# Optimization experiments

Measured on AMD Instinct MI355X. Metric: run time of the kernel, lower is better.

Reference implementation:

```python
import jax, jax.numpy as jnp
import numpy as np

N, E, EE = 1024, 32768, 262144
C_S, C_Z, C_G, H, R = 384, 128, 16, 4, 64
EPS = 1e-8


def _rbf(d, D_count=R, D_min=0.0, D_max=20.0):
    # gvp-style radial basis: exp(-((d - mu)/sigma)^2), mu in linspace(D_min, D_max)
    mu = jnp.linspace(D_min, D_max, D_count, dtype=d.dtype)
    sigma = (D_max - D_min) / D_count
    return jnp.exp(-(((d[..., None] - mu) / sigma) ** 2))


def _layernorm(x, g, b, eps=1e-5):
    m = jnp.mean(x, axis=-1, keepdims=True)
    v = jnp.var(x, axis=-1, keepdims=True)
    return (x - m) * jax.lax.rsqrt(v + eps) * g + b


def setup_inputs() -> dict:
    key = jax.random.key(0)
    ks = jax.random.split(key, 32)
    s = 0.02
    inp = {
        'node_features': jax.random.normal(ks[0], (N, C_S), jnp.float32),
        'node_trans': jax.random.normal(ks[1], (N, 3), jnp.float32) * 10.0,
        'edge_features': jax.random.normal(ks[2], (E, C_Z), jnp.float32),
        'edge_index': jax.random.randint(ks[3], (2, E), 0, N),
        'edge_edge_index': jax.random.randint(ks[4], (2, EE), 0, E),
        # layer norm
        'ln_g': jnp.ones((C_Z,), jnp.float32),
        'ln_b': jnp.zeros((C_Z,), jnp.float32),
        # node_left / node_right
        'W_nl': jax.random.normal(ks[5], (C_S, C_G), jnp.float32) * s,
        'b_nl': jnp.zeros((C_G,), jnp.float32),
        'W_nr': jax.random.normal(ks[6], (C_S, C_G), jnp.float32) * s,
        'b_nr': jnp.zeros((C_G,), jnp.float32),
        # bias_gate: (c_gate_s^2 -> c_z)
        'W_bg': jax.random.normal(ks[7], (C_G * C_G, C_Z), jnp.float32) * s,
        'b_bg': jnp.zeros((C_Z,), jnp.float32),
        # dist_bias: (num_rbf -> c_z)
        'W_db': jax.random.normal(ks[8], (R, C_Z), jnp.float32) * s,
        'b_db': jnp.zeros((C_Z,), jnp.float32),
        # to_bias: (c_z -> num_heads), no bias
        'W_tb': jax.random.normal(ks[9], (C_Z, H), jnp.float32) * s,
        # q / kv
        'W_q': jax.random.normal(ks[10], (C_Z, C_Z), jnp.float32) * s,
        'b_q': jnp.zeros((C_Z,), jnp.float32),
        'W_kv': jax.random.normal(ks[11], (C_Z, 2 * C_Z), jnp.float32) * s,
        'b_kv': jnp.zeros((2 * C_Z,), jnp.float32),
        # out gate + out proj
        'W_og': jax.random.normal(ks[12], (C_Z, C_Z), jnp.float32) * s,
        'b_og': jnp.zeros((C_Z,), jnp.float32),
        'W_out': jax.random.normal(ks[13], (C_Z, C_Z), jnp.float32) * s,
        'b_out': jnp.zeros((C_Z,), jnp.float32),
    }
    return inp


def reference(node_features, node_trans, edge_features, edge_index, edge_edge_index,
              ln_g, ln_b, W_nl, b_nl, W_nr, b_nr, W_bg, b_bg, W_db, b_db, W_tb,
              W_q, b_q, W_kv, b_kv, W_og, b_og, W_out, b_out):
    d = C_Z // H
    ee0, ee1 = edge_edge_index[0], edge_edge_index[1]
    # node indices of the two triangle corner nodes for each edge-edge pair
    n1 = edge_index[0, ee1]  # [EE]
    n2 = edge_index[0, ee0]  # [EE]

    ef = _layernorm(edge_features, ln_g, ln_b)  # [E, c_z]

    nl = node_features @ W_nl + b_nl  # [N, c_g]
    nr = node_features @ W_nr + b_nr
    # outer product gate features per edge-edge pair
    e3 = jnp.einsum('bi,bj->bij', nl[n1], nr[n2]).reshape(-1, C_G * C_G)  # [EE, c_g^2]
    gate = e3 @ W_bg + b_bg  # [EE, c_z]

    dist = jnp.linalg.norm(node_trans[n1] - node_trans[n2] + EPS, axis=-1)  # [EE]
    dist_bias = _rbf(dist) @ W_db + b_db  # [EE, c_z]
    bias = (jax.nn.sigmoid(gate) * dist_bias) @ W_tb  # [EE, H]

    q = (ef @ W_q + b_q).reshape(E, H, d)
    kv = ef @ W_kv + b_kv
    k = kv[:, :C_Z].reshape(E, H, d)
    v = kv[:, C_Z:].reshape(E, H, d)

    attn = jnp.einsum('bhi,bhi->bh', q[ee1], k[ee0]) * (1.0 / np.sqrt(C_Z)) + bias  # [EE, H]

    # segment softmax over target edge ee1
    seg_max = jax.ops.segment_max(attn, ee1, num_segments=E)  # [E, H]
    p = jnp.exp(attn - seg_max[ee1])
    seg_sum = jax.ops.segment_sum(p, ee1, num_segments=E)
    p = p / (seg_sum[ee1] + 1e-16)

    upd = jax.ops.segment_sum(v[ee0] * p[..., None], ee1, num_segments=E)  # [E, H, d]
    upd = upd.reshape(E, C_Z)
    upd = upd * jax.nn.sigmoid(ef @ W_og + b_og)
    return upd @ W_out + b_out
```

## Files before the change

kernel.cpp:

```cpp
#include <hip/hip_runtime.h>
#include <math.h>

#define NN 1024
#define NE 32768
#define NEE 262144
#define CS 384
#define CZ 128
#define CG 16
#define NH 4
#define NR 64

typedef __attribute__((ext_vector_type(8))) short short8v;
typedef __attribute__((ext_vector_type(4))) float f32x4;
typedef unsigned short ushort_t;

__device__ __forceinline__ float sigmoidf_(float x) { return 1.0f / (1.0f + __expf(-x)); }

__device__ __forceinline__ ushort_t f2bf(float x) {
    union { float f; unsigned u; } v; v.f = x;
    unsigned r = v.u + 0x7fff + ((v.u >> 16) & 1);
    return (ushort_t)(r >> 16);
}
__device__ __forceinline__ float bf2f(ushort_t x) {
    union { unsigned u; float f; } v; v.u = ((unsigned)x) << 16;
    return v.f;
}

__global__ void node_proj_kernel(const float* __restrict__ nf,
                                 const float* __restrict__ Wl, const float* __restrict__ bl,
                                 const float* __restrict__ Wr, const float* __restrict__ br,
                                 ushort_t* __restrict__ nl16, float* __restrict__ nr) {
    int wave = threadIdx.x >> 6, lane = threadIdx.x & 63;
    int n = blockIdx.x * 4 + wave;
    if (lane >= 32) return;
    bool isl = lane < 16;
    int o = isl ? lane : lane - 16;
    const float* W = isl ? Wl : Wr;
    float acc = isl ? bl[o] : br[o];
    const float* x = nf + n * CS;
    for (int k = 0; k < CS; ++k) acc += x[k] * W[k * 16 + o];
    if (isl) nl16[n * 16 + o] = f2bf(acc);
    else     nr[n * 16 + o] = acc;
}

__global__ void build_Tt_kernel(const float* __restrict__ nr, const float* __restrict__ Wbg,
                                ushort_t* __restrict__ Tbf) {
    int n = blockIdx.x;
    int t = threadIdx.x;
    int c = t & 127, i0 = t >> 7;
    __shared__ float nrs[16];
    if (t < 16) nrs[t] = nr[n * 16 + t];
    __syncthreads();
    for (int i = i0; i < 16; i += 2) {
        float acc = 0.f;
#pragma unroll
        for (int j = 0; j < 16; ++j) acc += nrs[j] * Wbg[(i * 16 + j) * 128 + c];
        Tbf[n * 2048 + c * 16 + i] = f2bf(acc);
    }
}

__global__ void ln_kernel(const float* __restrict__ x, const float* __restrict__ g,
                          const float* __restrict__ b, ushort_t* __restrict__ ef) {
    int wave = threadIdx.x >> 6, lane = threadIdx.x & 63;
    int e = blockIdx.x * 4 + wave;
    int c0 = lane, c1 = lane + 64;
    float x0 = x[e * 128 + c0], x1 = x[e * 128 + c1];
    float s = x0 + x1;
#pragma unroll
    for (int m = 1; m < 64; m <<= 1) s += __shfl_xor(s, m);
    float mean = s * (1.f / 128.f);
    float d0 = x0 - mean, d1 = x1 - mean;
    float v = d0 * d0 + d1 * d1;
#pragma unroll
    for (int m = 1; m < 64; m <<= 1) v += __shfl_xor(v, m);
    v *= (1.f / 128.f);
    float inv = rsqrtf(v + 1e-5f);
    ef[e * 128 + c0] = f2bf(d0 * inv * g[c0] + b[c0]);
    ef[e * 128 + c1] = f2bf(d1 * inv * g[c1] + b[c1]);
}

__global__ void prep_w_kernel(const float* __restrict__ Wq, const float* __restrict__ bq,
                              const float* __restrict__ Wkv, const float* __restrict__ bkv,
                              const float* __restrict__ Wog, const float* __restrict__ bog,
                              const float* __restrict__ Wdb, const float* __restrict__ Wout,
                              ushort_t* __restrict__ WcatT, float* __restrict__ bcat,
                              ushort_t* __restrict__ WdbT, ushort_t* __restrict__ WoutT) {
    int idx = blockIdx.x * 256 + threadIdx.x;
    int col = idx >> 7, k = idx & 127;
    float w;
    if (col < 128) w = Wq[k * 128 + col];
    else if (col < 256) w = Wog[k * 128 + (col - 128)];
    else if (col < 384) w = Wkv[k * 256 + (col - 256)];
    else w = Wkv[k * 256 + 128 + (col - 384)];
    WcatT[idx] = f2bf(w);
    if (idx < 512) {
        float bb;
        if (idx < 128) bb = bq[idx];
        else if (idx < 256) bb = bog[idx - 128];
        else if (idx < 384) bb = bkv[idx - 256];
        else bb = bkv[idx - 384 + 128];
        bcat[idx] = bb;
    }
    if (idx < 128 * 64) {
        int c = idx >> 6, r = idx & 63;
        WdbT[idx] = f2bf(Wdb[r * 128 + c]);
    }
    if (idx < 128 * 128) {
        int c = idx >> 7, kk = idx & 127;
        WoutT[idx] = f2bf(Wout[kk * 128 + c]);
    }
}

__global__ void __launch_bounds__(256) mfma_gemm_proj(const ushort_t* __restrict__ Abf,
                                                      const ushort_t* __restrict__ Bt,
                                                      const float* __restrict__ bias,
                                                      ushort_t* __restrict__ qog,
                                                      ushort_t* __restrict__ kvo) {
    __shared__ ushort_t As[128][136];
    __shared__ ushort_t Bs[64][136];
    int t = threadIdx.x;
    int row0 = blockIdx.y * 128;
    int n0 = blockIdx.x * 64;
#pragma unroll
    for (int u = 0; u < 8; ++u) {
        int idx = t + u * 256;
        int r = idx >> 4, seg = idx & 15;
        *(short8v*)&As[r][seg * 8] = *(const short8v*)&Abf[(size_t)(row0 + r) * 128 + seg * 8];
    }
#pragma unroll
    for (int u = 0; u < 4; ++u) {
        int idx = t + u * 256;
        int r = idx >> 4, seg = idx & 15;
        *(short8v*)&Bs[r][seg * 8] = *(const short8v*)&Bt[(size_t)(n0 + r) * 128 + seg * 8];
    }
    __syncthreads();
    int lane = t & 63, w = t >> 6;
    int wr = (w >> 1) * 64, wc = (w & 1) * 32;
    int fr = lane & 15, fk = (lane >> 4) * 8;
    f32x4 acc[4][2] = {};
#pragma unroll
    for (int kk = 0; kk < 4; ++kk) {
        short8v a[4], b[2];
#pragma unroll
        for (int m = 0; m < 4; ++m) a[m] = *(const short8v*)&As[wr + m * 16 + fr][kk * 32 + fk];
#pragma unroll
        for (int n = 0; n < 2; ++n) b[n] = *(const short8v*)&Bs[wc + n * 16 + fr][kk * 32 + fk];
#pragma unroll
        for (int m = 0; m < 4; ++m)
#pragma unroll
            for (int n = 0; n < 2; ++n)
                acc[m][n] = __builtin_amdgcn_mfma_f32_16x16x32_bf16(a[m], b[n], acc[m][n], 0, 0, 0);
    }
    __syncthreads();
    ushort_t (*stage)[72] = (ushort_t(*)[72])&As[0][0];
    int orow = (lane >> 4) * 4;
#pragma unroll
    for (int m = 0; m < 4; ++m)
#pragma unroll
        for (int n = 0; n < 2; ++n) {
            int col = wc + n * 16 + fr;
            float bv = bias[n0 + col];
#pragma unroll
            for (int j = 0; j < 4; ++j)
                stage[wr + m * 16 + orow + j][col] = f2bf(acc[m][n][j] + bv);
        }
    __syncthreads();
    ushort_t* basep; int cbase;
    if (n0 < 256) { basep = qog; cbase = n0; } else { basep = kvo; cbase = n0 - 256; }
#pragma unroll
    for (int u = 0; u < 4; ++u) {
        int idx = t + u * 256;
        int r = idx >> 3, seg = idx & 7;
        *(short8v*)&basep[(size_t)(row0 + r) * 256 + cbase + seg * 8] = *(const short8v*)&stage[r][seg * 8];
    }
}

__global__ void __launch_bounds__(256) mfma_gemm_out(const float* __restrict__ Af,
                                                     const ushort_t* __restrict__ Bt,
                                                     const float* __restrict__ bias,
                                                     float* __restrict__ out) {
    __shared__ ushort_t As[128][136];
    __shared__ ushort_t Bs[64][136];
    int t = threadIdx.x;
    int row0 = blockIdx.y * 128;
    int n0 = blockIdx.x * 64;
#pragma unroll
    for (int u = 0; u < 8; ++u) {
        int idx = t + u * 256;
        int r = idx >> 4, seg = idx & 15;
        float4 f0 = *(const float4*)&Af[(size_t)(row0 + r) * 128 + seg * 8];
        float4 f1 = *(const float4*)&Af[(size_t)(row0 + r) * 128 + seg * 8 + 4];
        short8v pk;
        pk[0] = (short)f2bf(f0.x); pk[1] = (short)f2bf(f0.y);
        pk[2] = (short)f2bf(f0.z); pk[3] = (short)f2bf(f0.w);
        pk[4] = (short)f2bf(f1.x); pk[5] = (short)f2bf(f1.y);
        pk[6] = (short)f2bf(f1.z); pk[7] = (short)f2bf(f1.w);
        *(short8v*)&As[r][seg * 8] = pk;
    }
#pragma unroll
    for (int u = 0; u < 4; ++u) {
        int idx = t + u * 256;
        int r = idx >> 4, seg = idx & 15;
        *(short8v*)&Bs[r][seg * 8] = *(const short8v*)&Bt[(size_t)(n0 + r) * 128 + seg * 8];
    }
    __syncthreads();
    int lane = t & 63, w = t >> 6;
    int wr = (w >> 1) * 64, wc = (w & 1) * 32;
    int fr = lane & 15, fk = (lane >> 4) * 8;
    f32x4 acc[4][2] = {};
#pragma unroll
    for (int kk = 0; kk < 4; ++kk) {
        short8v a[4], b[2];
#pragma unroll
        for (int m = 0; m < 4; ++m) a[m] = *(const short8v*)&As[wr + m * 16 + fr][kk * 32 + fk];
#pragma unroll
        for (int n = 0; n < 2; ++n) b[n] = *(const short8v*)&Bs[wc + n * 16 + fr][kk * 32 + fk];
#pragma unroll
        for (int m = 0; m < 4; ++m)
#pragma unroll
            for (int n = 0; n < 2; ++n)
                acc[m][n] = __builtin_amdgcn_mfma_f32_16x16x32_bf16(a[m], b[n], acc[m][n], 0, 0, 0);
    }
    __syncthreads();
    float (*stage)[68] = (float(*)[68])&As[0][0];
    int orow = (lane >> 4) * 4;
#pragma unroll
    for (int m = 0; m < 4; ++m)
#pragma unroll
        for (int n = 0; n < 2; ++n) {
            int col = wc + n * 16 + fr;
            float bv = bias[n0 + col];
#pragma unroll
            for (int j = 0; j < 4; ++j)
                stage[wr + m * 16 + orow + j][col] = acc[m][n][j] + bv;
        }
    __syncthreads();
#pragma unroll
    for (int u = 0; u < 8; ++u) {
        int idx = t + u * 256;
        int r = idx >> 4, c4 = idx & 15;
        *(float4*)&out[(size_t)(row0 + r) * 128 + n0 + c4 * 4] = *(const float4*)&stage[r][c4 * 4];
    }
}

__global__ void hist_kernel(const int* __restrict__ eei, const int* __restrict__ ei,
                            int* __restrict__ cnt, int* __restrict__ cnt2) {
    int p = blockIdx.x * 256 + threadIdx.x;
    int e0 = eei[p], e1 = eei[NEE + p];
    atomicAdd(&cnt[e1], 1);
    atomicAdd(&cnt2[ei[e0]], 1);
}

__global__ void scan_kernel(const int* __restrict__ cnt, int* __restrict__ offs,
                            int* __restrict__ cursor) {
    __shared__ int part[1024];
    int t = threadIdx.x;
    int loc[32];
    int s = 0;
#pragma unroll
    for (int j = 0; j < 32; ++j) { loc[j] = cnt[t * 32 + j]; s += loc[j]; }
    part[t] = s;
    __syncthreads();
    for (int d = 1; d < 1024; d <<= 1) {
        int add = (t >= d) ? part[t - d] : 0;
        __syncthreads();
        part[t] += add;
        __syncthreads();
    }
    int excl = (t == 0) ? 0 : part[t - 1];
#pragma unroll
    for (int j = 0; j < 32; ++j) {
        offs[t * 32 + j] = excl;
        cursor[t * 32 + j] = excl;
        excl += loc[j];
    }
    if (t == 1023) offs[NE] = excl;
}

__global__ void scan2_kernel(const int* __restrict__ cnt2, int* __restrict__ offs2,
                             int* __restrict__ cursor2) {
    __shared__ int part[256];
    int t = threadIdx.x;
    int loc[4];
    int s = 0;
#pragma unroll
    for (int j = 0; j < 4; ++j) { loc[j] = cnt2[t * 4 + j]; s += loc[j]; }
    part[t] = s;
    __syncthreads();
    for (int d = 1; d < 256; d <<= 1) {
        int add = (t >= d) ? part[t - d] : 0;
        __syncthreads();
        part[t] += add;
        __syncthreads();
    }
    int excl = (t == 0) ? 0 : part[t - 1];
#pragma unroll
    for (int j = 0; j < 4; ++j) {
        offs2[t * 4 + j] = excl;
        cursor2[t * 4 + j] = excl;
        excl += loc[j];
    }
    if (t == 255) offs2[1024] = excl;
}

__global__ void scatter_both_kernel(const int* __restrict__ eei, const int* __restrict__ ei,
                                    int* __restrict__ cursor, int* __restrict__ csr,
                                    int* __restrict__ cursor2, int* __restrict__ csr2) {
    int p = blockIdx.x * 256 + threadIdx.x;
    int e1 = eei[NEE + p];
    int pos = atomicAdd(&cursor[e1], 1);
    csr[pos] = p;
    int n2 = ei[eei[p]];
    int pos2 = atomicAdd(&cursor2[n2], 1);
    csr2[pos2] = p;
}

__global__ void __launch_bounds__(256) bias_kernel(
    const int* __restrict__ csr2, const int* __restrict__ offs2,
    const int* __restrict__ eei, const int* __restrict__ ei,
    const ushort_t* __restrict__ nl16, const ushort_t* __restrict__ Tbf,
    const ushort_t* __restrict__ WdbT, const float* __restrict__ ntr,
    const float* __restrict__ bbg, const float* __restrict__ bdb,
    const float* __restrict__ Wtb, float* __restrict__ bias_p) {
    __shared__ ushort_t Tt[128 * 24];
    __shared__ ushort_t Wd[128 * 72];
    int t = threadIdx.x;
    int n2 = blockIdx.x;
    {
        const ushort_t* src = Tbf + n2 * 2048;
        int c = t >> 1, hh = t & 1;
        *(int4*)&Tt[c * 24 + hh * 8] = *(const int4*)&src[c * 16 + hh * 8];
    }
#pragma unroll
    for (int u = 0; u < 4; ++u) {
        int idx = t + u * 256;
        int c = idx >> 3, seg = idx & 7;
        *(int4*)&Wd[c * 72 + seg * 8] = *(const int4*)&WdbT[c * 64 + seg * 8];
    }
    __syncthreads();

    int lane = t & 63, w = t >> 6;
    int cl = lane & 15, g = lane >> 4;
    float wtb[8][4], bdbl[8], bbgl[8];
#pragma unroll
    for (int nb = 0; nb < 8; ++nb) {
        int c = nb * 16 + cl;
        float4 wt = *(const float4*)&Wtb[c * 4];
        wtb[nb][0] = wt.x; wtb[nb][1] = wt.y; wtb[nb][2] = wt.z; wtb[nb][3] = wt.w;
        bdbl[nb] = bdb[c];
        bbgl[nb] = bbg[c];
    }
    float px2 = ntr[n2 * 3 + 0], py2 = ntr[n2 * 3 + 1], pz2 = ntr[n2 * 3 + 2];
    int bstart = offs2[n2], bend = offs2[n2 + 1];
    const float MU = 20.0f / 63.0f;

    for (int base = bstart + w * 16; base < bend; base += 64) {
        int idx = base + cl;
        int ip = (idx < bend) ? idx : (bend - 1);
        int p = csr2[ip];
        int e1 = eei[NEE + p];
        int n1 = ei[e1];
        short8v aNL = {0, 0, 0, 0, 0, 0, 0, 0};
        if (g < 2) aNL = *(const short8v*)&nl16[n1 * 16 + g * 8];
        float dx = ntr[n1 * 3 + 0] - px2 + 1e-8f;
        float dy = ntr[n1 * 3 + 1] - py2 + 1e-8f;
        float dz = ntr[n1 * 3 + 2] - pz2 + 1e-8f;
        float d = sqrtf(dx * dx + dy * dy + dz * dz);
        short8v ea, eb;
#pragma unroll
        for (int j = 0; j < 8; ++j) {
            float r = (float)(g * 8 + j);
            float t0 = (d - r * MU) * 3.2f;
            float t1 = (d - (r + 32.0f) * MU) * 3.2f;
            ea[j] = (short)f2bf(__expf(-t0 * t0));
            eb[j] = (short)f2bf(__expf(-t1 * t1));
        }
        float bacc[4][4] = {};
        f32x4 zero4 = {0.f, 0.f, 0.f, 0.f};
#pragma unroll
        for (int nb = 0; nb < 8; ++nb) {
            int c = nb * 16 + cl;
            short8v bT = {0, 0, 0, 0, 0, 0, 0, 0};
            if (g < 2) bT = *(const short8v*)&Tt[c * 24 + g * 8];
            f32x4 G = __builtin_amdgcn_mfma_f32_16x16x32_bf16(aNL, bT, zero4, 0, 0, 0);
            short8v bW0 = *(const short8v*)&Wd[c * 72 + g * 8];
            short8v bW1 = *(const short8v*)&Wd[c * 72 + 32 + g * 8];
            f32x4 D = __builtin_amdgcn_mfma_f32_16x16x32_bf16(ea, bW0, zero4, 0, 0, 0);
            D = __builtin_amdgcn_mfma_f32_16x16x32_bf16(eb, bW1, D, 0, 0, 0);
#pragma unroll
            for (int j = 0; j < 4; ++j) {
                float gv = G[j] + bbgl[nb];
                float db = D[j] + bdbl[nb];
                float s = db * sigmoidf_(gv);
                bacc[j][0] += s * wtb[nb][0];
                bacc[j][1] += s * wtb[nb][1];
                bacc[j][2] += s * wtb[nb][2];
                bacc[j][3] += s * wtb[nb][3];
            }
        }
#pragma unroll
        for (int j = 0; j < 4; ++j)
#pragma unroll
            for (int h = 0; h < 4; ++h) {
                float v = bacc[j][h];
                v += __shfl_xor(v, 1);
                v += __shfl_xor(v, 2);
                v += __shfl_xor(v, 4);
                v += __shfl_xor(v, 8);
                bacc[j][h] = v;
            }
        int row = g * 4 + (cl >> 2), h = cl & 3;
        int oidx = base + row;
        if (oidx < bend) {
            int pp = csr2[oidx];
            bias_p[pp * 4 + h] = bacc[cl >> 2][h];
        }
    }
}

__global__ void __launch_bounds__(256) segment_kernel(const ushort_t* __restrict__ qog,
                                                      const ushort_t* __restrict__ kv,
                                                      const float* __restrict__ bias_p,
                                                      const int* __restrict__ offs,
                                                      const int* __restrict__ csr,
                                                      const int* __restrict__ eei,
                                                      float* __restrict__ updg) {
    int t = threadIdx.x, wave = t >> 6, lane = t & 63;
    int gw = blockIdx.x * 4 + wave;
    int c0 = lane, c1 = lane + 64;
    int h0 = lane >> 5, h1 = 2 + (lane >> 5);
    const float scale = 0.08838834764831845f;
    for (int it = 0; it < 4; ++it) {
        int e = gw * 4 + it;
        int st = offs[e], en = offs[e + 1];
        float q0 = bf2f(qog[(size_t)e * 256 + c0]);
        float q1 = bf2f(qog[(size_t)e * 256 + c1]);
        float s0 = 0.f, s1 = 0.f, u0 = 0.f, u1 = 0.f;
        for (int idx = st; idx < en; ++idx) {
            int p = csr[idx];
            int e0 = eei[p];
            const ushort_t* kvr = kv + (size_t)e0 * 256;
            float k0 = bf2f(kvr[c0]), k1 = bf2f(kvr[c1]);
            float v0 = bf2f(kvr[128 + c0]), v1 = bf2f(kvr[128 + c1]);
            float ta = q0 * k0, tb = q1 * k1;
#pragma unroll
            for (int m = 1; m < 32; m <<= 1) { ta += __shfl_xor(ta, m); tb += __shfl_xor(tb, m); }
            float bh0 = bias_p[p * 4 + h0], bh1 = bias_p[p * 4 + h1];
            float w0 = __expf(ta * scale + bh0);
            float w1 = __expf(tb * scale + bh1);
            s0 += w0; u0 += w0 * v0;
            s1 += w1; u1 += w1 * v1;
        }
        u0 /= (s0 + 1e-16f);
        u1 /= (s1 + 1e-16f);
        u0 *= sigmoidf_(bf2f(qog[(size_t)e * 256 + 128 + c0]));
        u1 *= sigmoidf_(bf2f(qog[(size_t)e * 256 + 128 + c1]));
        updg[(size_t)e * 128 + c0] = u0;
        updg[(size_t)e * 128 + c1] = u1;
    }
}

extern "C" void kernel_launch(void* const* d_in, const int* in_sizes, int n_in,
                              void* d_out, int out_size, void* d_ws, size_t ws_size,
                              hipStream_t stream) {
    const float* node_features = (const float*)d_in[0];
    const float* node_trans   = (const float*)d_in[1];
    const float* edge_features= (const float*)d_in[2];
    const int*   edge_index   = (const int*)d_in[3];
    const int*   eei          = (const int*)d_in[4];
    const float* ln_g  = (const float*)d_in[5];
    const float* ln_b  = (const float*)d_in[6];
    const float* W_nl  = (const float*)d_in[7];
    const float* b_nl  = (const float*)d_in[8];
    const float* W_nr  = (const float*)d_in[9];
    const float* b_nr  = (const float*)d_in[10];
    const float* W_bg  = (const float*)d_in[11];
    const float* b_bg  = (const float*)d_in[12];
    const float* W_db  = (const float*)d_in[13];
    const float* b_db  = (const float*)d_in[14];
    const float* W_tb  = (const float*)d_in[15];
    const float* W_q   = (const float*)d_in[16];
    const float* b_q   = (const float*)d_in[17];
    const float* W_kv  = (const float*)d_in[18];
    const float* b_kv  = (const float*)d_in[19];
    const float* W_og  = (const float*)d_in[20];
    const float* b_og  = (const float*)d_in[21];
    const float* W_out = (const float*)d_in[22];
    const float* b_out = (const float*)d_in[23];
    float* out = (float*)d_out;

    char* ws = (char*)d_ws;
    size_t off = 0;
    auto alloc = [&](size_t bytes) -> void* {
        void* p = ws + off;
        off += (bytes + 255) & ~(size_t)255;
        return p;
    };
    ushort_t* nl16  = (ushort_t*)alloc((size_t)NN * 16 * 2);
    float*    nr    = (float*)alloc((size_t)NN * 16 * 4);
    ushort_t* Tbf   = (ushort_t*)alloc((size_t)NN * 2048 * 2);
    ushort_t* WdbT  = (ushort_t*)alloc((size_t)128 * 64 * 2);
    ushort_t* WcatT = (ushort_t*)alloc((size_t)512 * 128 * 2);
    float*    bcat  = (float*)alloc((size_t)512 * 4);
    ushort_t* WoutT = (ushort_t*)alloc((size_t)128 * 128 * 2);
    ushort_t* ef_bf = (ushort_t*)alloc((size_t)NE * 128 * 2);
    ushort_t* qog   = (ushort_t*)alloc((size_t)NE * 256 * 2);
    ushort_t* kvb   = (ushort_t*)alloc((size_t)NE * 256 * 2);
    float*    bias_p= (float*)alloc((size_t)NEE * 4 * 4);
    float*    updg  = (float*)alloc((size_t)NE * 128 * 4);
    int*      cnt   = (int*)alloc((size_t)NE * 4);
    int*      cnt2  = (int*)alloc((size_t)1024 * 4);
    int*      offs  = (int*)alloc((size_t)(NE + 1) * 4);
    int*      offs2 = (int*)alloc((size_t)1025 * 4);
    int*      cursor  = (int*)alloc((size_t)NE * 4);
    int*      cursor2 = (int*)alloc((size_t)1024 * 4);
    int*      csr   = (int*)alloc((size_t)NEE * 4);
    int*      csr2  = (int*)alloc((size_t)NEE * 4);

    hipMemsetAsync(cnt, 0, (size_t)NE * 4 + 1024 * 4, stream);

    node_proj_kernel<<<NN / 4, 256, 0, stream>>>(node_features, W_nl, b_nl, W_nr, b_nr, nl16, nr);
    build_Tt_kernel<<<NN, 256, 0, stream>>>(nr, W_bg, Tbf);
    ln_kernel<<<NE / 4, 256, 0, stream>>>(edge_features, ln_g, ln_b, ef_bf);
    prep_w_kernel<<<256, 256, 0, stream>>>(W_q, b_q, W_kv, b_kv, W_og, b_og, W_db, W_out,
                                           WcatT, bcat, WdbT, WoutT);
    mfma_gemm_proj<<<dim3(8, 256), 256, 0, stream>>>(ef_bf, WcatT, bcat, qog, kvb);
    hist_kernel<<<NEE / 256, 256, 0, stream>>>(eei, edge_index, cnt, cnt2);
    scan_kernel<<<1, 1024, 0, stream>>>(cnt, offs, cursor);
    scan2_kernel<<<1, 256, 0, stream>>>(cnt2, offs2, cursor2);
    scatter_both_kernel<<<NEE / 256, 256, 0, stream>>>(eei, edge_index, cursor, csr, cursor2, csr2);
    bias_kernel<<<NN, 256, 0, stream>>>(csr2, offs2, eei, edge_index, nl16, Tbf, WdbT,
                                        node_trans, b_bg, b_db, W_tb, bias_p);
    segment_kernel<<<NE / 16, 256, 0, stream>>>(qog, kvb, bias_p, offs, csr, eei, updg);
    mfma_gemm_out<<<dim3(2, 256), 256, 0, stream>>>(updg, WoutT, b_out, out);
}
```

Baseline: 447.4 us.

## Precompute per-pair n1/distance at scatter, split bias blocks, head-local segment reductions

The scatter kernel now stores, in csr2 order, each pair's source node and its node distance, so the bias kernel no longer chases eei→edge_index→node_trans per pair. The bias kernel launches four blocks per target node, each taking a strided quarter of that node's pairs. This raises parallelism, at the cost of loading the shared T and W tiles four times. The segment kernel now gives each lane two adjacent channels of a single head, using 32-bit packed bf16 loads, a 16-lane shuffle reduction, one exp per lane and float2 stores.

```diff
diff --git a/kernel.cpp b/kernel.cpp
--- a/kernel.cpp
+++ b/kernel.cpp
@@ -304,28 +304,37 @@
 }
 
 __global__ void scatter_both_kernel(const int* __restrict__ eei, const int* __restrict__ ei,
+                                    const float* __restrict__ ntr,
                                     int* __restrict__ cursor, int* __restrict__ csr,
-                                    int* __restrict__ cursor2, int* __restrict__ csr2) {
+                                    int* __restrict__ cursor2, int* __restrict__ csr2,
+                                    int* __restrict__ n1rank, float* __restrict__ drank) {
     int p = blockIdx.x * 256 + threadIdx.x;
-    int e1 = eei[NEE + p];
+    int e0 = eei[p], e1 = eei[NEE + p];
     int pos = atomicAdd(&cursor[e1], 1);
     csr[pos] = p;
-    int n2 = ei[eei[p]];
+    int n1 = ei[e1], n2 = ei[e0];
     int pos2 = atomicAdd(&cursor2[n2], 1);
     csr2[pos2] = p;
-}
-
+    n1rank[pos2] = n1;
+    float dx = ntr[n1 * 3 + 0] - ntr[n2 * 3 + 0] + 1e-8f;
+    float dy = ntr[n1 * 3 + 1] - ntr[n2 * 3 + 1] + 1e-8f;
+    float dz = ntr[n1 * 3 + 2] - ntr[n2 * 3 + 2] + 1e-8f;
+    drank[pos2] = sqrtf(dx * dx + dy * dy + dz * dz);
+}
+
+#define BSPLIT 4
 __global__ void __launch_bounds__(256) bias_kernel(
     const int* __restrict__ csr2, const int* __restrict__ offs2,
-    const int* __restrict__ eei, const int* __restrict__ ei,
+    const int* __restrict__ n1rank, const float* __restrict__ drank,
     const ushort_t* __restrict__ nl16, const ushort_t* __restrict__ Tbf,
-    const ushort_t* __restrict__ WdbT, const float* __restrict__ ntr,
+    const ushort_t* __restrict__ WdbT,
     const float* __restrict__ bbg, const float* __restrict__ bdb,
     const float* __restrict__ Wtb, float* __restrict__ bias_p) {
     __shared__ ushort_t Tt[128 * 24];
     __shared__ ushort_t Wd[128 * 72];
     int t = threadIdx.x;
-    int n2 = blockIdx.x;
+    int n2 = blockIdx.x >> 2;
+    int s  = blockIdx.x & 3;
     {
         const ushort_t* src = Tbf + n2 * 2048;
         int c = t >> 1, hh = t & 1;
@@ -350,22 +359,16 @@
         bdbl[nb] = bdb[c];
         bbgl[nb] = bbg[c];
     }
-    float px2 = ntr[n2 * 3 + 0], py2 = ntr[n2 * 3 + 1], pz2 = ntr[n2 * 3 + 2];
     int bstart = offs2[n2], bend = offs2[n2 + 1];
     const float MU = 20.0f / 63.0f;
 
-    for (int base = bstart + w * 16; base < bend; base += 64) {
+    for (int base = bstart + (s * 4 + w) * 16; base < bend; base += 16 * 4 * BSPLIT) {
         int idx = base + cl;
         int ip = (idx < bend) ? idx : (bend - 1);
-        int p = csr2[ip];
-        int e1 = eei[NEE + p];
-        int n1 = ei[e1];
+        int n1 = n1rank[ip];
+        float d = drank[ip];
         short8v aNL = {0, 0, 0, 0, 0, 0, 0, 0};
         if (g < 2) aNL = *(const short8v*)&nl16[n1 * 16 + g * 8];
-        float dx = ntr[n1 * 3 + 0] - px2 + 1e-8f;
-        float dy = ntr[n1 * 3 + 1] - py2 + 1e-8f;
-        float dz = ntr[n1 * 3 + 2] - pz2 + 1e-8f;
-        float d = sqrtf(dx * dx + dy * dy + dz * dz);
         short8v ea, eb;
 #pragma unroll
         for (int j = 0; j < 8; ++j) {
@@ -391,11 +394,11 @@
             for (int j = 0; j < 4; ++j) {
                 float gv = G[j] + bbgl[nb];
                 float db = D[j] + bdbl[nb];
-                float s = db * sigmoidf_(gv);
-                bacc[j][0] += s * wtb[nb][0];
-                bacc[j][1] += s * wtb[nb][1];
-                bacc[j][2] += s * wtb[nb][2];
-                bacc[j][3] += s * wtb[nb][3];
+                float sg = db * sigmoidf_(gv);
+                bacc[j][0] += sg * wtb[nb][0];
+                bacc[j][1] += sg * wtb[nb][1];
+                bacc[j][2] += sg * wtb[nb][2];
+                bacc[j][3] += sg * wtb[nb][3];
             }
         }
 #pragma unroll
@@ -427,36 +430,34 @@
                                                       float* __restrict__ updg) {
     int t = threadIdx.x, wave = t >> 6, lane = t & 63;
     int gw = blockIdx.x * 4 + wave;
-    int c0 = lane, c1 = lane + 64;
-    int h0 = lane >> 5, h1 = 2 + (lane >> 5);
+    int h = lane >> 4;
     const float scale = 0.08838834764831845f;
     for (int it = 0; it < 4; ++it) {
         int e = gw * 4 + it;
         int st = offs[e], en = offs[e + 1];
-        float q0 = bf2f(qog[(size_t)e * 256 + c0]);
-        float q1 = bf2f(qog[(size_t)e * 256 + c1]);
-        float s0 = 0.f, s1 = 0.f, u0 = 0.f, u1 = 0.f;
+        unsigned qw = *(const unsigned*)&qog[(size_t)e * 256 + 2 * lane];
+        float q0 = bf2f((ushort_t)(qw & 0xffff)), q1 = bf2f((ushort_t)(qw >> 16));
+        float s = 0.f, u0 = 0.f, u1 = 0.f;
         for (int idx = st; idx < en; ++idx) {
             int p = csr[idx];
             int e0 = eei[p];
             const ushort_t* kvr = kv + (size_t)e0 * 256;
-            float k0 = bf2f(kvr[c0]), k1 = bf2f(kvr[c1]);
-            float v0 = bf2f(kvr[128 + c0]), v1 = bf2f(kvr[128 + c1]);
-            float ta = q0 * k0, tb = q1 * k1;
-#pragma unroll
-            for (int m = 1; m < 32; m <<= 1) { ta += __shfl_xor(ta, m); tb += __shfl_xor(tb, m); }
-            float bh0 = bias_p[p * 4 + h0], bh1 = bias_p[p * 4 + h1];
-            float w0 = __expf(ta * scale + bh0);
-            float w1 = __expf(tb * scale + bh1);
-            s0 += w0; u0 += w0 * v0;
-            s1 += w1; u1 += w1 * v1;
+            unsigned kw = *(const unsigned*)&kvr[2 * lane];
+            unsigned vw = *(const unsigned*)&kvr[128 + 2 * lane];
+            float ta = q0 * bf2f((ushort_t)(kw & 0xffff)) + q1 * bf2f((ushort_t)(kw >> 16));
+#pragma unroll
+            for (int m = 1; m < 16; m <<= 1) ta += __shfl_xor(ta, m);
+            float wgt = __expf(ta * scale + bias_p[p * 4 + h]);
+            s += wgt;
+            u0 += wgt * bf2f((ushort_t)(vw & 0xffff));
+            u1 += wgt * bf2f((ushort_t)(vw >> 16));
         }
-        u0 /= (s0 + 1e-16f);
-        u1 /= (s1 + 1e-16f);
-        u0 *= sigmoidf_(bf2f(qog[(size_t)e * 256 + 128 + c0]));
-        u1 *= sigmoidf_(bf2f(qog[(size_t)e * 256 + 128 + c1]));
-        updg[(size_t)e * 128 + c0] = u0;
-        updg[(size_t)e * 128 + c1] = u1;
+        float inv = 1.0f / (s + 1e-16f);
+        unsigned ogw = *(const unsigned*)&qog[(size_t)e * 256 + 128 + 2 * lane];
+        u0 = u0 * inv * sigmoidf_(bf2f((ushort_t)(ogw & 0xffff)));
+        u1 = u1 * inv * sigmoidf_(bf2f((ushort_t)(ogw >> 16)));
+        float2 uo; uo.x = u0; uo.y = u1;
+        *(float2*)&updg[(size_t)e * 128 + 2 * lane] = uo;
     }
 }
 
@@ -516,6 +517,8 @@
     int*      cursor2 = (int*)alloc((size_t)1024 * 4);
     int*      csr   = (int*)alloc((size_t)NEE * 4);
     int*      csr2  = (int*)alloc((size_t)NEE * 4);
+    int*      n1rank= (int*)alloc((size_t)NEE * 4);
+    float*    drank = (float*)alloc((size_t)NEE * 4);
 
     hipMemsetAsync(cnt, 0, (size_t)NE * 4 + 1024 * 4, stream);
 
@@ -528,9 +531,10 @@
     hist_kernel<<<NEE / 256, 256, 0, stream>>>(eei, edge_index, cnt, cnt2);
     scan_kernel<<<1, 1024, 0, stream>>>(cnt, offs, cursor);
     scan2_kernel<<<1, 256, 0, stream>>>(cnt2, offs2, cursor2);
-    scatter_both_kernel<<<NEE / 256, 256, 0, stream>>>(eei, edge_index, cursor, csr, cursor2, csr2);
-    bias_kernel<<<NN, 256, 0, stream>>>(csr2, offs2, eei, edge_index, nl16, Tbf, WdbT,
-                                        node_trans, b_bg, b_db, W_tb, bias_p);
+    scatter_both_kernel<<<NEE / 256, 256, 0, stream>>>(eei, edge_index, node_trans,
+                                                       cursor, csr, cursor2, csr2, n1rank, drank);
+    bias_kernel<<<NN * BSPLIT, 256, 0, stream>>>(csr2, offs2, n1rank, drank, nl16, Tbf, WdbT,
+                                                 b_bg, b_db, W_tb, bias_p);
     segment_kernel<<<NE / 16, 256, 0, stream>>>(qog, kvb, bias_p, offs, csr, eei, updg);
     mfma_gemm_out<<<dim3(2, 256), 256, 0, stream>>>(updg, WoutT, b_out, out);
 }
```

Result: no change. 452.3 us (+1.1%).
